# Kernel tuning notes

Measured on AMD Instinct MI355X. Metric: run time of the kernel, lower is better.

## Reference

```python
import jax, jax.numpy as jnp
import numpy as np

DF, DK, DG, NR = 1024, 64, 64, 16
DV = DF // NR  # 64
N = 1024       # num_rois


def setup_inputs() -> dict:
    key = jax.random.key(0)
    ks = jax.random.split(key, 12)
    def xavier(k, out_d, in_d):
        lim = float(np.sqrt(6.0 / (in_d + out_d)))
        return jax.random.uniform(k, (out_d, in_d), jnp.float32, -lim, lim)
    return {
        "x": jax.random.normal(ks[0], (N, DF), jnp.float32),
        "position_embedding": jax.random.uniform(ks[1], (N, N, DG), jnp.float32),
        "Wq": xavier(ks[2], DK * NR, DF), "bq": jnp.zeros((DK * NR,), jnp.float32),
        "Wk": xavier(ks[3], DK * NR, DF), "bk": jnp.zeros((DK * NR,), jnp.float32),
        "Wv": xavier(ks[4], DF, DF),     "bv": jnp.zeros((DF,), jnp.float32),
        "Wg": xavier(ks[5], NR, DG),     "bg": jnp.zeros((NR,), jnp.float32),
        "Wy": xavier(ks[6], DF, DF),     "by": jnp.zeros((DF,), jnp.float32),
    }


def reference(x, position_embedding, Wq, bq, Wk, bk, Wv, bv, Wg, bg, Wy, by):
    n = x.shape[0]
    # geometry bias: linear -> relu -> clamp_min(1e-6) -> log, then head-major
    g = jnp.einsum('ijd,hd->hij', position_embedding, Wg) + bg[:, None, None]  # [Nr, N, N]
    g = jnp.log(jnp.maximum(jax.nn.relu(g), 1e-6))
    # projections, reshaped to [Nr, N, d]
    Q = (x @ Wq.T + bq).reshape(n, NR, DK).transpose(1, 0, 2)   # [Nr, N, dk]
    K = (x @ Wk.T + bk).reshape(n, NR, DK).transpose(1, 0, 2)   # [Nr, N, dk]
    V = (x @ Wv.T + bv).reshape(n, NR, DV).transpose(1, 0, 2)   # [Nr, N, dv]
    scores = jnp.einsum('hnd,hmd->hnm', Q, K) + g               # no 1/sqrt(dk) scaling (faithful)
    attn = jax.nn.softmax(scores, axis=2)
    Y = jnp.einsum('hnm,hmd->hnd', attn, V)                      # [Nr, N, dv]
    Y = Y.transpose(1, 0, 2).reshape(n, DF)
    y = Y @ Wy.T + by
    return x + y
```

## Files before the change

### kernel.cpp

```cpp
#include <hip/hip_runtime.h>
#include <hip/hip_bf16.h>


typedef __bf16 bf16_t;
typedef _Float16 f16_t;
typedef __attribute__((ext_vector_type(8))) __bf16 bf16x8;
typedef __attribute__((ext_vector_type(8))) _Float16 f16x8;
typedef __attribute__((ext_vector_type(4))) float f32x4;

__device__ inline bf16_t f2b(float f) {
    unsigned u = __builtin_bit_cast(unsigned, f);
    unsigned r = u + 0x7fffu + ((u >> 16) & 1u);
    unsigned short h = (unsigned short)(r >> 16);
    return __builtin_bit_cast(bf16_t, h);
}

__global__ __launch_bounds__(256) void fused_g_proj_k(
        const float* __restrict__ pe, const float* __restrict__ Wg, const float* __restrict__ bg,
        f16_t* __restrict__ Wout,
        const float* __restrict__ x,
        const float* __restrict__ Wq, const float* __restrict__ bq, bf16_t* __restrict__ Qb,
        const float* __restrict__ Wk, const float* __restrict__ bk, bf16_t* __restrict__ Kb,
        const float* __restrict__ Wv, const float* __restrict__ bv, bf16_t* __restrict__ Vb) {
    __shared__ float4 tile4[64][16];
    __shared__ bf16_t As[2][64][40];
    __shared__ bf16_t Bs[2][64][40];
    const int bid = blockIdx.x;
    const int t = threadIdx.x;

    if (bid < 768) {
        const int z = bid >> 8, rem = bid & 255;
        const float* B = (z == 0) ? Wq : (z == 1) ? Wk : Wv;
        const float* bias = (z == 0) ? bq : (z == 1) ? bk : bv;
        bf16_t* outp = (z == 0) ? Qb : (z == 1) ? Kb : Vb;
        const int m0 = (rem >> 4) * 64, n0 = (rem & 15) * 64;
        const int lr = t >> 2, lq = t & 3;

        auto stage = [&](bf16_t (*dst)[64][40], const float* __restrict__ Sp, int row0, int buf, int k0) {
            const float* p = Sp + (long)(row0 + lr) * 1024 + k0 + lq * 8;
            float4 u0 = *(const float4*)p;
            float4 u1 = *(const float4*)(p + 4);
            bf16x8 v;
            v[0] = f2b(u0.x); v[1] = f2b(u0.y); v[2] = f2b(u0.z); v[3] = f2b(u0.w);
            v[4] = f2b(u1.x); v[5] = f2b(u1.y); v[6] = f2b(u1.z); v[7] = f2b(u1.w);
            *(bf16x8*)&dst[buf][lr][lq * 8] = v;
        };

        const int wid = t >> 6, lane = t & 63;
        const int wm = (wid >> 1) * 32, wn = (wid & 1) * 32;
        const int ml = lane & 15, kl = (lane >> 4) * 8;
        f32x4 acc[2][2] = {};

        stage(As, x, m0, 0, 0);
        stage(Bs, B, n0, 0, 0);
        __syncthreads();
        for (int kt = 0; kt < 32; kt++) {
            const int buf = kt & 1;
            if (kt + 1 < 32) { stage(As, x, m0, buf ^ 1, (kt + 1) * 32); stage(Bs, B, n0, buf ^ 1, (kt + 1) * 32); }
            bf16x8 a0 = *(const bf16x8*)&As[buf][wm + ml][kl];
            bf16x8 a1 = *(const bf16x8*)&As[buf][wm + 16 + ml][kl];
            bf16x8 b0 = *(const bf16x8*)&Bs[buf][wn + ml][kl];
            bf16x8 b1 = *(const bf16x8*)&Bs[buf][wn + 16 + ml][kl];
            acc[0][0] = __builtin_amdgcn_mfma_f32_16x16x32_bf16(a0, b0, acc[0][0], 0, 0, 0);
            acc[0][1] = __builtin_amdgcn_mfma_f32_16x16x32_bf16(a0, b1, acc[0][1], 0, 0, 0);
            acc[1][0] = __builtin_amdgcn_mfma_f32_16x16x32_bf16(a1, b0, acc[1][0], 0, 0, 0);
            acc[1][1] = __builtin_amdgcn_mfma_f32_16x16x32_bf16(a1, b1, acc[1][1], 0, 0, 0);
            __syncthreads();
        }

#pragma unroll
        for (int mt = 0; mt < 2; mt++)
#pragma unroll
            for (int nt = 0; nt < 2; nt++) {
                f32x4 v = acc[mt][nt];
                const int rbase = m0 + wm + mt * 16 + ((lane >> 4) << 2);
                const int col = n0 + wn + nt * 16 + (lane & 15);
#pragma unroll
                for (int r = 0; r < 4; r++) {
                    const int row = rbase + r;
                    float val = v[r] + bias[col];
                    int h = col >> 6, d = col & 63;
                    if (z < 2) outp[((long)h << 16) + ((long)row << 6) + d] = f2b(val);
                    else       outp[((long)h << 16) + ((long)d << 10) + row] = f2b(val);
                }
            }
    } else {
        const long rowbase = (long)(bid - 768) * 64;
        const float4* src = (const float4*)(pe + rowbase * 64);
#pragma unroll
        for (int p = 0; p < 4; p++) {
            float4 v = src[p * 256 + t];
            int fi = p * 256 + t;
            int r = fi >> 4, c = fi & 15;
            tile4[r][c ^ (r & 15)] = v;
        }
        __syncthreads();
        const int lane = t & 63;
        float4 pv[16];
#pragma unroll
        for (int i = 0; i < 16; i++) pv[i] = tile4[lane][i ^ (lane & 15)];
        const int hq = __builtin_amdgcn_readfirstlane((t >> 6) << 2);
        for (int p = 0; p < 4; p++) {
            const int hh = __builtin_amdgcn_readfirstlane(hq + p);
            const float* wgp = Wg + (hh << 6);
            float a = bg[hh];
#pragma unroll
            for (int i = 0; i < 16; i++) {
                float4 w = *(const float4*)(wgp + i * 4);
                a += pv[i].x * w.x + pv[i].y * w.y + pv[i].z * w.z + pv[i].w * w.w;
            }
            Wout[((long)hh << 20) + rowbase + lane] = (f16_t)fmaxf(a, 1e-6f);
        }
    }
}

__global__ __launch_bounds__(256) void gemmY_k(const bf16_t* __restrict__ A,
                                               const float* __restrict__ Bw,
                                               const float* __restrict__ bias,
                                               float* __restrict__ outp,
                                               const float* __restrict__ extra) {
    __shared__ bf16_t As[2][64][40];
    __shared__ bf16_t Bs[2][64][40];
    const int t = threadIdx.x;
    const int m0 = blockIdx.y * 64, n0 = blockIdx.x * 64;
    const int lr = t >> 2, lq = t & 3;

    auto stageA = [&](int buf, int k0) {
        const bf16_t* p = A + (long)(m0 + lr) * 1024 + k0 + lq * 8;
        *(bf16x8*)&As[buf][lr][lq * 8] = *(const bf16x8*)p;
    };
    auto stageB = [&](int buf, int k0) {
        const float* p = Bw + (long)(n0 + lr) * 1024 + k0 + lq * 8;
        float4 u0 = *(const float4*)p;
        float4 u1 = *(const float4*)(p + 4);
        bf16x8 v;
        v[0] = f2b(u0.x); v[1] = f2b(u0.y); v[2] = f2b(u0.z); v[3] = f2b(u0.w);
        v[4] = f2b(u1.x); v[5] = f2b(u1.y); v[6] = f2b(u1.z); v[7] = f2b(u1.w);
        *(bf16x8*)&Bs[buf][lr][lq * 8] = v;
    };

    const int wid = t >> 6, lane = t & 63;
    const int wm = (wid >> 1) * 32, wn = (wid & 1) * 32;
    const int ml = lane & 15, kl = (lane >> 4) * 8;
    f32x4 acc[2][2] = {};

    stageA(0, 0);
    stageB(0, 0);
    __syncthreads();
    for (int kt = 0; kt < 32; kt++) {
        const int buf = kt & 1;
        if (kt + 1 < 32) { stageA(buf ^ 1, (kt + 1) * 32); stageB(buf ^ 1, (kt + 1) * 32); }
        bf16x8 a0 = *(const bf16x8*)&As[buf][wm + ml][kl];
        bf16x8 a1 = *(const bf16x8*)&As[buf][wm + 16 + ml][kl];
        bf16x8 b0 = *(const bf16x8*)&Bs[buf][wn + ml][kl];
        bf16x8 b1 = *(const bf16x8*)&Bs[buf][wn + 16 + ml][kl];
        acc[0][0] = __builtin_amdgcn_mfma_f32_16x16x32_bf16(a0, b0, acc[0][0], 0, 0, 0);
        acc[0][1] = __builtin_amdgcn_mfma_f32_16x16x32_bf16(a0, b1, acc[0][1], 0, 0, 0);
        acc[1][0] = __builtin_amdgcn_mfma_f32_16x16x32_bf16(a1, b0, acc[1][0], 0, 0, 0);
        acc[1][1] = __builtin_amdgcn_mfma_f32_16x16x32_bf16(a1, b1, acc[1][1], 0, 0, 0);
        __syncthreads();
    }

#pragma unroll
    for (int mt = 0; mt < 2; mt++)
#pragma unroll
        for (int nt = 0; nt < 2; nt++) {
            f32x4 v = acc[mt][nt];
            const int rbase = m0 + wm + mt * 16 + ((lane >> 4) << 2);
            const int col = n0 + wn + nt * 16 + (lane & 15);
#pragma unroll
            for (int r = 0; r < 4; r++) {
                const int row = rbase + r;
                long idx = ((long)row << 10) + col;
                outp[idx] = v[r] + bias[col] + extra[idx];
            }
        }
}

__global__ __launch_bounds__(256) void attn_kernel(const bf16_t* __restrict__ Q,
                                                   const bf16_t* __restrict__ K,
                                                   const bf16_t* __restrict__ Vt,
                                                   const f16_t* __restrict__ Wf,
                                                   bf16_t* __restrict__ Y) {
    __shared__ bf16_t Qs[64][72];
    __shared__ bf16_t Ks[2][64][72];
    __shared__ bf16_t Vts[2][64][72];
    __shared__ f16_t  Ws[2][64][72];
    __shared__ bf16_t Ps[4][16][72];

    const int qt = blockIdx.x, h = blockIdx.y;
    const int t = threadIdx.x;
    const int w = t >> 6, lane = t & 63;
    const int ml = lane & 15, kq = lane >> 4;
    const int q0 = qt << 6;
    const int sr = t >> 2, sc = (t & 3) << 4;

    const bf16_t* Kh = K + ((long)h << 16);
    const bf16_t* Vh = Vt + ((long)h << 16);
    const f16_t*  Wh = Wf + ((long)h << 20) + ((long)(q0 + sr) << 10);

    {
        const bf16_t* src = Q + ((long)h << 16) + ((long)(q0 + sr) << 6) + sc;
        *(bf16x8*)&Qs[sr][sc]     = *(const bf16x8*)src;
        *(bf16x8*)&Qs[sr][sc + 8] = *(const bf16x8*)(src + 8);
        const bf16_t* ks = Kh + ((long)sr << 6) + sc;
        *(bf16x8*)&Ks[0][sr][sc]     = *(const bf16x8*)ks;
        *(bf16x8*)&Ks[0][sr][sc + 8] = *(const bf16x8*)(ks + 8);
        const bf16_t* vs = Vh + ((long)sr << 10) + sc;
        *(bf16x8*)&Vts[0][sr][sc]     = *(const bf16x8*)vs;
        *(bf16x8*)&Vts[0][sr][sc + 8] = *(const bf16x8*)(vs + 8);
        const f16_t* gs = Wh + sc;
        *(f16x8*)&Ws[0][sr][sc]     = *(const f16x8*)gs;
        *(f16x8*)&Ws[0][sr][sc + 8] = *(const f16x8*)(gs + 8);
    }
    __syncthreads();

    const bf16x8 aq0 = *(const bf16x8*)&Qs[(w << 4) + ml][kq * 8];
    const bf16x8 aq1 = *(const bf16x8*)&Qs[(w << 4) + ml][32 + kq * 8];

    f32x4 O[4] = {};
    float lsum[4] = {0.f, 0.f, 0.f, 0.f};

    int buf = 0;
    for (int kt = 0; kt < 16; kt++) {
        bf16x8 rk0, rk1, rv0, rv1;
        f16x8 rw0, rw1;
        const bool pf = (kt < 15);
        if (pf) {
            const int k0 = (kt + 1) << 6;
            const bf16_t* ks = Kh + ((long)(k0 + sr) << 6) + sc;
            rk0 = *(const bf16x8*)ks; rk1 = *(const bf16x8*)(ks + 8);
            const bf16_t* vs = Vh + ((long)sr << 10) + k0 + sc;
            rv0 = *(const bf16x8*)vs; rv1 = *(const bf16x8*)(vs + 8);
            const f16_t* gs = Wh + k0 + sc;
            rw0 = *(const f16x8*)gs; rw1 = *(const f16x8*)(gs + 8);
        }

        f32x4 s[4] = {};
#pragma unroll
        for (int c = 0; c < 4; c++) {
            bf16x8 bk0 = *(const bf16x8*)&Ks[buf][(c << 4) + ml][kq * 8];
            bf16x8 bk1 = *(const bf16x8*)&Ks[buf][(c << 4) + ml][32 + kq * 8];
            s[c] = __builtin_amdgcn_mfma_f32_16x16x32_bf16(aq0, bk0, s[c], 0, 0, 0);
            s[c] = __builtin_amdgcn_mfma_f32_16x16x32_bf16(aq1, bk1, s[c], 0, 0, 0);
        }
#pragma unroll
        for (int c = 0; c < 4; c++) {
#pragma unroll
            for (int r = 0; r < 4; r++) {
                float wv = (float)Ws[buf][(w << 4) + (kq << 2) + r][(c << 4) + ml];
                float p = __expf(s[c][r]) * wv;
                lsum[r] += p;
                Ps[w][(kq << 2) + r][(c << 4) + ml] = f2b(p);
            }
        }
        const bf16x8 pa0 = *(const bf16x8*)&Ps[w][ml][kq * 8];
        const bf16x8 pa1 = *(const bf16x8*)&Ps[w][ml][32 + kq * 8];
#pragma unroll
        for (int c = 0; c < 4; c++) {
            bf16x8 v0 = *(const bf16x8*)&Vts[buf][(c << 4) + ml][kq * 8];
            bf16x8 v1 = *(const bf16x8*)&Vts[buf][(c << 4) + ml][32 + kq * 8];
            O[c] = __builtin_amdgcn_mfma_f32_16x16x32_bf16(pa0, v0, O[c], 0, 0, 0);
            O[c] = __builtin_amdgcn_mfma_f32_16x16x32_bf16(pa1, v1, O[c], 0, 0, 0);
        }

        if (pf) {
            const int nb = buf ^ 1;
            *(bf16x8*)&Ks[nb][sr][sc]      = rk0;
            *(bf16x8*)&Ks[nb][sr][sc + 8]  = rk1;
            *(bf16x8*)&Vts[nb][sr][sc]     = rv0;
            *(bf16x8*)&Vts[nb][sr][sc + 8] = rv1;
            *(f16x8*)&Ws[nb][sr][sc]       = rw0;
            *(f16x8*)&Ws[nb][sr][sc + 8]   = rw1;
        }
        __syncthreads();
        buf ^= 1;
    }

#pragma unroll
    for (int r = 0; r < 4; r++) {
        float v = lsum[r];
        v += __shfl_xor(v, 1); v += __shfl_xor(v, 2);
        v += __shfl_xor(v, 4); v += __shfl_xor(v, 8);
        lsum[r] = 1.0f / v;
    }
    const int rowb = q0 + (w << 4) + (kq << 2);
    const int colb = (h << 6) + ml;
#pragma unroll
    for (int c = 0; c < 4; c++)
#pragma unroll
        for (int r = 0; r < 4; r++)
            Y[((long)(rowb + r) << 10) + colb + (c << 4)] = f2b(O[c][r] * lsum[r]);
}

extern "C" void kernel_launch(void* const* d_in, const int* in_sizes, int n_in,
                              void* d_out, int out_size, void* d_ws, size_t ws_size,
                              hipStream_t stream) {
    const float* x  = (const float*)d_in[0];
    const float* pe = (const float*)d_in[1];
    const float* Wq = (const float*)d_in[2];
    const float* bq = (const float*)d_in[3];
    const float* Wk = (const float*)d_in[4];
    const float* bk = (const float*)d_in[5];
    const float* Wv = (const float*)d_in[6];
    const float* bv = (const float*)d_in[7];
    const float* Wg = (const float*)d_in[8];
    const float* bg = (const float*)d_in[9];
    const float* Wy = (const float*)d_in[10];
    const float* by = (const float*)d_in[11];

    char* ws = (char*)d_ws;
    f16_t*  Wf = (f16_t*)ws;
    bf16_t* Qb = (bf16_t*)(ws + (32ul << 20));
    bf16_t* Kb = (bf16_t*)(ws + (34ul << 20));
    bf16_t* Vb = (bf16_t*)(ws + (36ul << 20));
    bf16_t* Yb = (bf16_t*)(ws + (38ul << 20));

    fused_g_proj_k<<<768 + 16384, 256, 0, stream>>>(pe, Wg, bg, Wf,
                                                    x, Wq, bq, Qb, Wk, bk, Kb, Wv, bv, Vb);
    attn_kernel<<<dim3(16, 16), 256, 0, stream>>>(Qb, Kb, Vb, Wf, Yb);
    gemmY_k<<<dim3(16, 16), 256, 0, stream>>>(Yb, Wy, by, (float*)d_out, x);
}
```

Before: 127.8 us.

## Process eight geometry chunks per block with register prefetch of next chunk

Geometry-projection blocks now each handle eight consecutive 64-row chunks of the position embedding instead of one, cutting that part of the grid from 16384 to 2048 blocks. While computing the current chunk from shared memory, each thread prefetches the next chunk into registers, then writes it to shared memory after a barrier. This amortizes block launch overhead and overlaps global loads with compute, at the cost of extra barriers, more register pressure, and fewer blocks to hide latency.

```diff
diff --git a/kernel.cpp b/kernel.cpp
--- a/kernel.cpp
+++ b/kernel.cpp
@@ -85,31 +85,56 @@
                 }
             }
     } else {
-        const long rowbase = (long)(bid - 768) * 64;
-        const float4* src = (const float4*)(pe + rowbase * 64);
-#pragma unroll
-        for (int p = 0; p < 4; p++) {
-            float4 v = src[p * 256 + t];
-            int fi = p * 256 + t;
-            int r = fi >> 4, c = fi & 15;
-            tile4[r][c ^ (r & 15)] = v;
+        const int gb = bid - 768;
+        const long chunk0 = (long)gb * 8;
+        const int lane = t & 63;
+        const int hq = (t >> 6) << 2;
+
+        {
+            const float4* src = (const float4*)(pe + chunk0 * 4096);
+#pragma unroll
+            for (int p = 0; p < 4; p++) {
+                float4 v = src[p * 256 + t];
+                int fi = p * 256 + t;
+                int r = fi >> 4, c = fi & 15;
+                tile4[r][c ^ (r & 15)] = v;
+            }
         }
         __syncthreads();
-        const int lane = t & 63;
-        float4 pv[16];
-#pragma unroll
-        for (int i = 0; i < 16; i++) pv[i] = tile4[lane][i ^ (lane & 15)];
-        const int hq = __builtin_amdgcn_readfirstlane((t >> 6) << 2);
-        for (int p = 0; p < 4; p++) {
-            const int hh = __builtin_amdgcn_readfirstlane(hq + p);
-            const float* wgp = Wg + (hh << 6);
-            float a = bg[hh];
-#pragma unroll
-            for (int i = 0; i < 16; i++) {
-                float4 w = *(const float4*)(wgp + i * 4);
-                a += pv[i].x * w.x + pv[i].y * w.y + pv[i].z * w.z + pv[i].w * w.w;
-            }
-            Wout[((long)hh << 20) + rowbase + lane] = (f16_t)fmaxf(a, 1e-6f);
+
+        for (int i = 0; i < 8; i++) {
+            float4 pf[4];
+            if (i < 7) {
+                const float4* src = (const float4*)(pe + (chunk0 + i + 1) * 4096);
+#pragma unroll
+                for (int p = 0; p < 4; p++) pf[p] = src[p * 256 + t];
+            }
+            float4 pv[16];
+#pragma unroll
+            for (int q = 0; q < 16; q++) pv[q] = tile4[lane][q ^ (lane & 15)];
+            const long rowbase = (chunk0 + i) * 64;
+#pragma unroll
+            for (int p = 0; p < 4; p++) {
+                const int hh = __builtin_amdgcn_readfirstlane(hq + p);
+                const float* wgp = Wg + (hh << 6);
+                float a = bg[hh];
+#pragma unroll
+                for (int q = 0; q < 16; q++) {
+                    float4 w = *(const float4*)(wgp + q * 4);
+                    a += pv[q].x * w.x + pv[q].y * w.y + pv[q].z * w.z + pv[q].w * w.w;
+                }
+                Wout[((long)hh << 20) + rowbase + lane] = (f16_t)fmaxf(a, 1e-6f);
+            }
+            __syncthreads();
+            if (i < 7) {
+#pragma unroll
+                for (int p = 0; p < 4; p++) {
+                    int fi = p * 256 + t;
+                    int r = fi >> 4, c = fi & 15;
+                    tile4[r][c ^ (r & 15)] = pf[p];
+                }
+                __syncthreads();
+            }
         }
     }
 }
@@ -316,8 +341,8 @@
     bf16_t* Vb = (bf16_t*)(ws + (36ul << 20));
     bf16_t* Yb = (bf16_t*)(ws + (38ul << 20));
 
-    fused_g_proj_k<<<768 + 16384, 256, 0, stream>>>(pe, Wg, bg, Wf,
-                                                    x, Wq, bq, Qb, Wk, bk, Kb, Wv, bv, Vb);
+    fused_g_proj_k<<<768 + 2048, 256, 0, stream>>>(pe, Wg, bg, Wf,
+                                                   x, Wq, bq, Qb, Wk, bk, Kb, Wv, bv, Vb);
     attn_kernel<<<dim3(16, 16), 256, 0, stream>>>(Qb, Kb, Vb, Wf, Yb);
     gemmY_k<<<dim3(16, 16), 256, 0, stream>>>(Yb, Wy, by, (float*)d_out, x);
 }
```

After: 175.9 us. +37.7%, slower.

## Compute geometry bias with per-thread row quarters and shuffle reduction instead of LDS transpose

Applied to the files above, without the earlier changes.

The geometry-bias branch stops staging position_embedding through a swizzled shared-memory tile with a barrier. Instead, each group of 4 threads splits one 64-wide row, computes partial dot products for all 16 heads, and combines them with xor shuffles. Each thread then writes 4 of the heads. This removes the LDS round trip and the __syncthreads, but adds redundant Wg loads per thread and 32 shuffles, and each store now writes to scattered head offsets.

```diff
diff --git a/kernel.cpp b/kernel.cpp
--- a/kernel.cpp
+++ b/kernel.cpp
@@ -22,7 +22,6 @@
         const float* __restrict__ Wq, const float* __restrict__ bq, bf16_t* __restrict__ Qb,
         const float* __restrict__ Wk, const float* __restrict__ bk, bf16_t* __restrict__ Kb,
         const float* __restrict__ Wv, const float* __restrict__ bv, bf16_t* __restrict__ Vb) {
-    __shared__ float4 tile4[64][16];
     __shared__ bf16_t As[2][64][40];
     __shared__ bf16_t Bs[2][64][40];
     const int bid = blockIdx.x;
@@ -86,30 +85,38 @@
             }
     } else {
         const long rowbase = (long)(bid - 768) * 64;
-        const float4* src = (const float4*)(pe + rowbase * 64);
-#pragma unroll
-        for (int p = 0; p < 4; p++) {
-            float4 v = src[p * 256 + t];
-            int fi = p * 256 + t;
-            int r = fi >> 4, c = fi & 15;
-            tile4[r][c ^ (r & 15)] = v;
-        }
-        __syncthreads();
-        const int lane = t & 63;
-        float4 pv[16];
-#pragma unroll
-        for (int i = 0; i < 16; i++) pv[i] = tile4[lane][i ^ (lane & 15)];
-        const int hq = __builtin_amdgcn_readfirstlane((t >> 6) << 2);
-        for (int p = 0; p < 4; p++) {
-            const int hh = __builtin_amdgcn_readfirstlane(hq + p);
-            const float* wgp = Wg + (hh << 6);
-            float a = bg[hh];
-#pragma unroll
-            for (int i = 0; i < 16; i++) {
-                float4 w = *(const float4*)(wgp + i * 4);
-                a += pv[i].x * w.x + pv[i].y * w.y + pv[i].z * w.z + pv[i].w * w.w;
-            }
-            Wout[((long)hh << 20) + rowbase + lane] = (f16_t)fmaxf(a, 1e-6f);
+        const int rr = t >> 2;
+        const int cq = t & 3;
+        const long row = rowbase + rr;
+
+        const float4* pr = (const float4*)(pe + (row << 6) + (cq << 4));
+        float4 pv0 = pr[0], pv1 = pr[1], pv2 = pr[2], pv3 = pr[3];
+
+        float p[16];
+#pragma unroll 4
+        for (int h = 0; h < 16; h++) {
+            const float4* wq = (const float4*)(Wg + (h << 6) + (cq << 4));
+            float4 w0 = wq[0], w1 = wq[1], w2 = wq[2], w3 = wq[3];
+            float a = pv0.x * w0.x + pv0.y * w0.y + pv0.z * w0.z + pv0.w * w0.w;
+            a += pv1.x * w1.x + pv1.y * w1.y + pv1.z * w1.z + pv1.w * w1.w;
+            a += pv2.x * w2.x + pv2.y * w2.y + pv2.z * w2.z + pv2.w * w2.w;
+            a += pv3.x * w3.x + pv3.y * w3.y + pv3.z * w3.z + pv3.w * w3.w;
+            p[h] = a;
+        }
+#pragma unroll
+        for (int h = 0; h < 16; h++) {
+            p[h] += __shfl_xor(p[h], 1);
+            p[h] += __shfl_xor(p[h], 2);
+        }
+        const float4 bg4 = *(const float4*)(bg + (cq << 2));
+#pragma unroll
+        for (int m = 0; m < 4; m++) {
+            float v = (cq & 2) ? ((cq & 1) ? p[12 + m] : p[8 + m])
+                               : ((cq & 1) ? p[4 + m]  : p[m]);
+            float bv_ = (m == 0) ? bg4.x : (m == 1) ? bg4.y : (m == 2) ? bg4.z : bg4.w;
+            v = fmaxf(v + bv_, 1e-6f);
+            const int h = (cq << 2) + m;
+            Wout[((long)h << 20) + rowbase + rr] = (f16_t)v;
         }
     }
 }
```

Result: slower. 390.8 us (+205.8%).

## Pipeline geometry-bias blocks with async global-to-LDS double buffering

Applied to the files above, without the earlier changes.

The geometry-bias part of the fused kernel now handles four 64-row chunks per block instead of one. It stages position-embedding tiles straight into LDS with global_load_lds, double-buffered and guarded by explicit vmcnt waits. Each wave computes its four heads in one pass over the tile, and the geometry blocks are moved ahead of the projection GEMM blocks in the grid. The aim is to cut block-launch overhead and hide the memory latency of streaming the 256MB embedding, at the cost of hand-tuned wait counts and a larger shared-memory footprint.

```diff
diff --git a/kernel.cpp b/kernel.cpp
--- a/kernel.cpp
+++ b/kernel.cpp
@@ -22,18 +22,79 @@
         const float* __restrict__ Wq, const float* __restrict__ bq, bf16_t* __restrict__ Qb,
         const float* __restrict__ Wk, const float* __restrict__ bk, bf16_t* __restrict__ Kb,
         const float* __restrict__ Wv, const float* __restrict__ bv, bf16_t* __restrict__ Vb) {
-    __shared__ float4 tile4[64][16];
-    __shared__ bf16_t As[2][64][40];
-    __shared__ bf16_t Bs[2][64][40];
+    __shared__ char smem_raw[32768];
     const int bid = blockIdx.x;
     const int t = threadIdx.x;
 
-    if (bid < 768) {
-        const int z = bid >> 8, rem = bid & 255;
+    if (bid < 4096) {
+        const long ch0 = (long)bid * 4;
+        const int w = t >> 6, lane = t & 63;
+        const int r = lane;
+        const int hq = w << 2;
+        float4* tile = (float4*)smem_raw;
+
+        auto stageg = [&](int buf, long ch) {
+#pragma unroll
+            for (int p = 0; p < 4; p++) {
+                int fi = p * 256 + t;
+                int rr = fi >> 4, cp = fi & 15, cc = cp ^ (rr & 15);
+                const float* gsrc = pe + (ch << 12) + (rr << 6) + (cc << 2);
+                float4* ldst = tile + buf * 1024 + p * 256 + (w << 6);
+                __builtin_amdgcn_global_load_lds((__attribute__((address_space(1))) const void*)gsrc,
+                                                 (__attribute__((address_space(3))) void*)ldst, 16, 0, 0);
+            }
+        };
+
+        stageg(0, ch0);
+        for (int i = 0; i < 4; i++) {
+            if (i < 3) stageg((i + 1) & 1, ch0 + i + 1);
+            if (i == 0)      asm volatile("s_waitcnt vmcnt(4)" ::: "memory");
+            else if (i < 3)  asm volatile("s_waitcnt vmcnt(8)" ::: "memory");
+            else             asm volatile("s_waitcnt vmcnt(4)" ::: "memory");
+            __builtin_amdgcn_s_barrier();
+            __builtin_amdgcn_sched_barrier(0);
+            const float4* tb = tile + (i & 1) * 1024 + (r << 4);
+            float a0 = 0.f, a1 = 0.f, a2 = 0.f, a3 = 0.f;
+#pragma unroll
+            for (int half = 0; half < 2; half++) {
+                float4 pv[8];
+#pragma unroll
+                for (int j = 0; j < 8; j++) {
+                    int c = half * 8 + j;
+                    pv[j] = tb[c ^ (r & 15)];
+                }
+                const float* wg0 = Wg + ((hq + 0) << 6) + (half << 5);
+                const float* wg1 = Wg + ((hq + 1) << 6) + (half << 5);
+                const float* wg2 = Wg + ((hq + 2) << 6) + (half << 5);
+                const float* wg3 = Wg + ((hq + 3) << 6) + (half << 5);
+#pragma unroll
+                for (int j = 0; j < 8; j++) {
+                    float4 w0 = *(const float4*)(wg0 + j * 4);
+                    float4 w1 = *(const float4*)(wg1 + j * 4);
+                    float4 w2 = *(const float4*)(wg2 + j * 4);
+                    float4 w3 = *(const float4*)(wg3 + j * 4);
+                    a0 += pv[j].x * w0.x + pv[j].y * w0.y + pv[j].z * w0.z + pv[j].w * w0.w;
+                    a1 += pv[j].x * w1.x + pv[j].y * w1.y + pv[j].z * w1.z + pv[j].w * w1.w;
+                    a2 += pv[j].x * w2.x + pv[j].y * w2.y + pv[j].z * w2.z + pv[j].w * w2.w;
+                    a3 += pv[j].x * w3.x + pv[j].y * w3.y + pv[j].z * w3.z + pv[j].w * w3.w;
+                }
+            }
+            const long rowg = ((ch0 + i) << 6) + r;
+            Wout[((long)(hq + 0) << 20) + rowg] = (f16_t)fmaxf(a0 + bg[hq + 0], 1e-6f);
+            Wout[((long)(hq + 1) << 20) + rowg] = (f16_t)fmaxf(a1 + bg[hq + 1], 1e-6f);
+            Wout[((long)(hq + 2) << 20) + rowg] = (f16_t)fmaxf(a2 + bg[hq + 2], 1e-6f);
+            Wout[((long)(hq + 3) << 20) + rowg] = (f16_t)fmaxf(a3 + bg[hq + 3], 1e-6f);
+            __builtin_amdgcn_s_barrier();
+        }
+    } else {
+        bf16_t (*As)[64][40] = (bf16_t(*)[64][40])smem_raw;
+        bf16_t (*Bs)[64][40] = (bf16_t(*)[64][40])(smem_raw + 10240);
+        const int rem = bid - 4096;
+        const int z = rem >> 8, rem2 = rem & 255;
         const float* B = (z == 0) ? Wq : (z == 1) ? Wk : Wv;
         const float* bias = (z == 0) ? bq : (z == 1) ? bk : bv;
         bf16_t* outp = (z == 0) ? Qb : (z == 1) ? Kb : Vb;
-        const int m0 = (rem >> 4) * 64, n0 = (rem & 15) * 64;
+        const int m0 = (rem2 >> 4) * 64, n0 = (rem2 & 15) * 64;
         const int lr = t >> 2, lq = t & 3;
 
         auto stage = [&](bf16_t (*dst)[64][40], const float* __restrict__ Sp, int row0, int buf, int k0) {
@@ -84,33 +145,6 @@
                     else       outp[((long)h << 16) + ((long)d << 10) + row] = f2b(val);
                 }
             }
-    } else {
-        const long rowbase = (long)(bid - 768) * 64;
-        const float4* src = (const float4*)(pe + rowbase * 64);
-#pragma unroll
-        for (int p = 0; p < 4; p++) {
-            float4 v = src[p * 256 + t];
-            int fi = p * 256 + t;
-            int r = fi >> 4, c = fi & 15;
-            tile4[r][c ^ (r & 15)] = v;
-        }
-        __syncthreads();
-        const int lane = t & 63;
-        float4 pv[16];
-#pragma unroll
-        for (int i = 0; i < 16; i++) pv[i] = tile4[lane][i ^ (lane & 15)];
-        const int hq = __builtin_amdgcn_readfirstlane((t >> 6) << 2);
-        for (int p = 0; p < 4; p++) {
-            const int hh = __builtin_amdgcn_readfirstlane(hq + p);
-            const float* wgp = Wg + (hh << 6);
-            float a = bg[hh];
-#pragma unroll
-            for (int i = 0; i < 16; i++) {
-                float4 w = *(const float4*)(wgp + i * 4);
-                a += pv[i].x * w.x + pv[i].y * w.y + pv[i].z * w.z + pv[i].w * w.w;
-            }
-            Wout[((long)hh << 20) + rowbase + lane] = (f16_t)fmaxf(a, 1e-6f);
-        }
     }
 }
 
@@ -316,8 +350,8 @@
     bf16_t* Vb = (bf16_t*)(ws + (36ul << 20));
     bf16_t* Yb = (bf16_t*)(ws + (38ul << 20));
 
-    fused_g_proj_k<<<768 + 16384, 256, 0, stream>>>(pe, Wg, bg, Wf,
-                                                    x, Wq, bq, Qb, Wk, bk, Kb, Wv, bv, Vb);
+    fused_g_proj_k<<<4096 + 768, 256, 0, stream>>>(pe, Wg, bg, Wf,
+                                                   x, Wq, bq, Qb, Wk, bk, Kb, Wv, bv, Vb);
     attn_kernel<<<dim3(16, 16), 256, 0, stream>>>(Qb, Kb, Vb, Wf, Yb);
     gemmY_k<<<dim3(16, 16), 256, 0, stream>>>(Yb, Wy, by, (float*)d_out, x);
 }
```

Result: slower. 228.6 us (+78.9%).
